# Kernel tuning notes

Measured on AMD Instinct MI355X. Metric: run time of the kernel, lower is better.

Reference implementation:

```python
import jax, jax.numpy as jnp
import numpy as np

NUM_HEAD = 16
MASKED_BIAS = -10000.0


def setup_inputs() -> dict:
    key = jax.random.key(0)
    k1, k2, k3 = jax.random.split(key, 3)
    B, M, N = 2, 2048, 1024
    x = jax.random.normal(k1, (B, M, N), dtype=jnp.float32)
    w_attn = jax.random.normal(k2, (N, 3 * N), dtype=jnp.float32) * 0.02
    w_proj = jax.random.normal(k3, (N, N), dtype=jnp.float32) * 0.02
    b_attn = jnp.zeros((3 * N,), dtype=jnp.float32)
    b_proj = jnp.zeros((N,), dtype=jnp.float32)
    return {"x": x, "w_attn": w_attn, "w_proj": w_proj,
            "b_attn": b_attn, "b_proj": b_proj}


def reference(x, w_attn, w_proj, b_attn, b_proj):
    B, M, N = x.shape
    H = NUM_HEAD
    d = N // H  # head dim
    # fused QKV projection: [B,M,3N]
    qkv = jnp.einsum('bmn,nd->bmd', x, w_attn) + b_attn
    q, k, v = jnp.split(qkv, 3, axis=-1)
    # split heads -> [B,H,M,d]
    q = q.reshape(B, M, H, d).transpose(0, 2, 1, 3)
    k = k.reshape(B, M, H, d).transpose(0, 2, 1, 3)
    v = v.reshape(B, M, H, d).transpose(0, 2, 1, 3)
    # scaled dot-product scores [B,H,M,M]
    scores = jnp.einsum('bhqd,bhkd->bhqk', q, k) / jnp.sqrt(jnp.float32(d))
    causal = jnp.tril(jnp.ones((M, M), dtype=bool))  # GPT-2 bias buffer
    scores = jnp.where(causal, scores, jnp.float32(MASKED_BIAS))
    attn = jax.nn.softmax(scores, axis=-1)
    # context [B,H,M,d] -> [B,M,N]
    ctx = jnp.einsum('bhqk,bhkd->bhqd', attn, v)
    ctx = ctx.transpose(0, 2, 1, 3).reshape(B, M, N)
    # output projection
    out = jnp.einsum('bmn,no->bmo', ctx, w_proj) + b_proj
    return out
```

## Files before the change

kernel.cpp:

```cpp
#include <hip/hip_runtime.h>

typedef __attribute__((ext_vector_type(8))) __bf16 bf16x8;
typedef __attribute__((ext_vector_type(4))) __bf16 bf16x4;
typedef __attribute__((ext_vector_type(4))) float f32x4;

__device__ __forceinline__ void async_copy16(const void* g, void* l) {
    __builtin_amdgcn_global_load_lds(
        (const __attribute__((address_space(1))) void*)g,
        (__attribute__((address_space(3))) void*)l, 16, 0, 0);
}

__global__ __launch_bounds__(256) void prep_k(
    const float* __restrict__ x, __bf16* __restrict__ xb,
    const float* __restrict__ wa, __bf16* __restrict__ wAt,
    const float* __restrict__ wp, __bf16* __restrict__ wPt)
{
    __shared__ float tile[32][33];
    const int bx = blockIdx.x;
    if (bx < 2048) {
        size_t i = ((size_t)bx * 256 + threadIdx.x) * 8;
        float4 a = *(const float4*)&x[i];
        float4 b = *(const float4*)&x[i + 4];
        bf16x8 o;
        o[0] = (__bf16)a.x; o[1] = (__bf16)a.y; o[2] = (__bf16)a.z; o[3] = (__bf16)a.w;
        o[4] = (__bf16)b.x; o[5] = (__bf16)b.y; o[6] = (__bf16)b.z; o[7] = (__bf16)b.w;
        *(bf16x8*)&xb[i] = o;
        return;
    }
    const float* src; __bf16* dst; int R, C, c0, r0;
    if (bx < 5120) {
        int id = bx - 2048;
        src = wa; dst = wAt; R = 1024; C = 3072;
        c0 = (id % 96) * 32; r0 = (id / 96) * 32;
    } else {
        int id = bx - 5120;
        src = wp; dst = wPt; R = 1024; C = 1024;
        c0 = (id & 31) * 32; r0 = (id >> 5) * 32;
    }
    int tx = threadIdx.x & 31, ty = threadIdx.x >> 5;
    for (int i = ty; i < 32; i += 8)
        tile[i][tx] = src[(size_t)(r0 + i) * C + (c0 + tx)];
    __syncthreads();
    for (int i = ty; i < 32; i += 8)
        dst[(size_t)(c0 + i) * R + (r0 + tx)] = (__bf16)tile[tx][i];
}

template <int MODE, int TN>
__global__ __launch_bounds__(256) void gemm_bt(
    const __bf16* __restrict__ A, const __bf16* __restrict__ Bt,
    const float* __restrict__ bias, int K,
    __bf16* __restrict__ O0, __bf16* __restrict__ O1, __bf16* __restrict__ O2,
    float* __restrict__ Of)
{
    constexpr int NJ = TN / 32;
    __shared__ __align__(16) __bf16 lds_a[2][128 * 32];
    __shared__ __align__(16) __bf16 lds_b[2][TN * 32];
    const int row0 = blockIdx.x * 128;
    const int col0 = blockIdx.y * TN;
    const int tid  = threadIdx.x;
    const int lane = tid & 63;
    const int w    = tid >> 6;
    const int wm   = (w >> 1) * 64, wn = (w & 1) * (TN / 2);
    const int quad = lane >> 4, l16 = lane & 15;

    auto stage = [&](int pb, int kb) {
#pragma unroll
        for (int t = 0; t < 2; ++t) {
            int s = t * 256 + tid;
            int L = s >> 3, c = (s & 7) ^ (L & 7);
            int row = 2 * L + (c >> 2), ch = c & 3;
            async_copy16(&A[(size_t)(row0 + row) * K + kb + ch * 8],
                         (char*)&lds_a[pb][0] + (t * 256 + w * 64) * 16);
        }
#pragma unroll
        for (int t = 0; t < TN / 64; ++t) {
            int s = t * 256 + tid;
            int L = s >> 3, c = (s & 7) ^ (L & 7);
            int row = 2 * L + (c >> 2), ch = c & 3;
            async_copy16(&Bt[(size_t)(col0 + row) * K + kb + ch * 8],
                         (char*)&lds_b[pb][0] + (t * 256 + w * 64) * 16);
        }
    };

    const int nIter = K >> 5;
    f32x4 acc[4][NJ] = {};
    stage(0, 0);
    for (int it = 0; it < nIter; ++it) {
        __syncthreads();
        if (it + 1 < nIter) stage((it + 1) & 1, (it + 1) << 5);
        const __bf16* la = &lds_a[it & 1][0];
        const __bf16* lb = &lds_b[it & 1][0];
        bf16x8 af[4], bfr[NJ];
#pragma unroll
        for (int i = 0; i < 4; ++i) {
            int r = wm + i * 16 + l16;
            int L = r >> 1, g = ((r & 1) * 4 + quad) ^ (L & 7);
            af[i] = *(const bf16x8*)&la[L * 64 + g * 8];
        }
#pragma unroll
        for (int j = 0; j < NJ; ++j) {
            int r = wn + j * 16 + l16;
            int L = r >> 1, g = ((r & 1) * 4 + quad) ^ (L & 7);
            bfr[j] = *(const bf16x8*)&lb[L * 64 + g * 8];
        }
#pragma unroll
        for (int i = 0; i < 4; ++i)
#pragma unroll
            for (int j = 0; j < NJ; ++j)
                acc[i][j] = __builtin_amdgcn_mfma_f32_16x16x32_bf16(
                    af[i], bfr[j], acc[i][j], 0, 0, 0);
    }

#pragma unroll
    for (int i = 0; i < 4; ++i) {
        int grow = row0 + wm + i * 16 + quad * 4;
#pragma unroll
        for (int j = 0; j < NJ; ++j) {
            int gcol = col0 + wn + j * 16 + l16;
            float bv = bias[gcol];
            if constexpr (MODE == 0) {
                int which = gcol >> 10;
                int n  = gcol & 1023;
                int hh = n >> 6, dd = n & 63;
                int bb = grow >> 11, mm0 = grow & 2047;
                int bhh = bb * 16 + hh;
                if (which == 2) {
                    int w64 = mm0 & 63;
                    int mi = (mm0 & ~63) | (w64 & 32) | ((w64 & 12) << 1)
                             | ((w64 & 16) >> 2);
                    bf16x4 pk;
#pragma unroll
                    for (int r = 0; r < 4; ++r)
                        pk[r] = (__bf16)(acc[i][j][r] + bv);
                    *(bf16x4*)&O2[((size_t)bhh * 64 + dd) * 2048 + mi] = pk;
                } else {
#pragma unroll
                    for (int r = 0; r < 4; ++r) {
                        float v = acc[i][j][r] + bv;
                        if (which == 0)
                            O0[((size_t)bhh * 2048 + mm0 + r) * 64 + dd] =
                                (__bf16)(v * 0.18033688011112042f);
                        else
                            O1[((size_t)bhh * 2048 + mm0 + r) * 64 + dd] =
                                (__bf16)v;
                    }
                }
            } else {
#pragma unroll
                for (int r = 0; r < 4; ++r) {
                    int gr = grow + r;
                    Of[(size_t)gr * 1024 + gcol] = acc[i][j][r] + bv;
                }
            }
        }
    }
}

__global__ __launch_bounds__(512, 4) void attn_kernel(
    const __bf16* __restrict__ Qh, const __bf16* __restrict__ Kh,
    const __bf16* __restrict__ Vt, __bf16* __restrict__ ctx)
{
    const int M = 2048, D = 64;
    const int bh = blockIdx.x;
    const int qt = 15 - blockIdx.y;
    const int b = bh >> 4, h = bh & 15;
    const int tid = threadIdx.x, lane = tid & 63, w = tid >> 6;
    const int quad = lane >> 4, l16 = lane & 15;

    const int q0 = qt * 128;
    const int nIter = 2 * qt + 2;

    __shared__ __align__(16) __bf16 smem[2][2][64 * 64];

    const __bf16* Qp = Qh + (size_t)bh * M * D;
    const __bf16* Kp = Kh + (size_t)bh * M * D;
    const __bf16* Vp = Vt + (size_t)bh * D * M;

    const int qw = q0 + w * 16;

    bf16x8 qf[2];
#pragma unroll
    for (int c = 0; c < 2; ++c)
        qf[c] = *(const bf16x8*)
            &Qp[(size_t)(qw + l16) * D + c * 32 + quad * 8];

    int ko[8];
#pragma unroll
    for (int t = 0; t < 4; ++t)
#pragma unroll
        for (int c = 0; c < 2; ++c) {
            int ch = ((c << 2) + quad) ^ (l16 & 7);
            ko[t * 2 + c] = (((t << 4) + l16) << 6) + (ch << 3);
        }
    int vo[8];
#pragma unroll
    for (int f = 0; f < 4; ++f)
#pragma unroll
        for (int tp = 0; tp < 2; ++tp) {
            int row = (f << 4) + l16;
            int g = ((tp << 2) + quad) ^ (row & 7);
            vo[f * 2 + tp] = (row << 6) + (g << 3);
        }

    const int cch = w * 64 + lane;
    const int srow = cch >> 3, sch = (cch & 7) ^ (srow & 7);
    const __bf16* kgp = &Kp[(size_t)srow * 64 + sch * 8];
    const __bf16* vgp = &Vp[(size_t)srow * M + sch * 8];
    char* const lbase = (char*)smem + w * 1024;

    auto stage = [&](int pb) {
        char* d = lbase + pb * 16384;
        async_copy16(kgp, d);
        async_copy16(vgp, d + 8192);
        kgp += 4096;
        vgp += 64;
    };

    f32x4 acc2[4] = {};
    f32x4 acc_s = {};
    const __bf16 onev = (__bf16)1.0f;
    const bf16x8 ones8 = {onev, onev, onev, onev, onev, onev, onev, onev};

    stage(0);

    for (int it = 0; it < nIter; ++it) {
        const int kb = it << 6;
        __syncthreads();
        if (it + 1 < nIter) stage((it + 1) & 1);
        if (kb > qw + 15) continue;
        const __bf16* kt = &smem[it & 1][0][0];
        const __bf16* vt = &smem[it & 1][1][0];

        f32x4 s[4];
        __builtin_amdgcn_s_setprio(1);
#pragma unroll
        for (int t = 0; t < 4; ++t) {
            f32x4 tt = {};
#pragma unroll
            for (int c = 0; c < 2; ++c) {
                bf16x8 kf = *(const bf16x8*)(kt + ko[t * 2 + c]);
                tt = __builtin_amdgcn_mfma_f32_16x16x32_bf16(
                    kf, qf[c], tt, 0, 0, 0);
            }
            s[t] = tt;
        }
        __builtin_amdgcn_s_setprio(0);
        if (kb + 63 > qw) {
#pragma unroll
            for (int t = 0; t < 4; ++t)
#pragma unroll
                for (int r = 0; r < 4; ++r)
                    if (kb + t * 16 + quad * 4 + r > qw + l16)
                        s[t][r] = -1e30f;
        }
        bf16x8 pf32[2];
#pragma unroll
        for (int tp = 0; tp < 2; ++tp) {
            bf16x8 pp;
#pragma unroll
            for (int r = 0; r < 4; ++r) {
                pp[r]     = (__bf16)exp2f(s[2 * tp][r]);
                pp[4 + r] = (__bf16)exp2f(s[2 * tp + 1][r]);
            }
            pf32[tp] = pp;
        }
        __builtin_amdgcn_s_setprio(1);
#pragma unroll
        for (int f = 0; f < 4; ++f) {
#pragma unroll
            for (int tp = 0; tp < 2; ++tp) {
                bf16x8 vv = *(const bf16x8*)(vt + vo[f * 2 + tp]);
                acc2[f] = __builtin_amdgcn_mfma_f32_16x16x32_bf16(
                    vv, pf32[tp], acc2[f], 0, 0, 0);
            }
        }
#pragma unroll
        for (int tp = 0; tp < 2; ++tp)
            acc_s = __builtin_amdgcn_mfma_f32_16x16x32_bf16(
                ones8, pf32[tp], acc_s, 0, 0, 0);
        __builtin_amdgcn_s_setprio(0);
    }

    __syncthreads();
    __bf16* ldsT = (__bf16*)smem;
    const float rinv = 1.0f / acc_s[0];
#pragma unroll
    for (int f = 0; f < 4; ++f) {
        bf16x4 ov;
#pragma unroll
        for (int r = 0; r < 4; ++r)
            ov[r] = (__bf16)(acc2[f][r] * rinv);
        *(bf16x4*)&ldsT[(w * 16 + l16) * 72 + f * 16 + quad * 4] = ov;
    }
    __syncthreads();
    {
        int qq = tid >> 2;
        int dp = (tid & 3) * 16;
        const __bf16* src = &ldsT[qq * 72 + dp];
        __bf16* dst = &ctx[((size_t)(b * 2048 + q0 + qq)) * 1024 + h * 64 + dp];
        *(bf16x8*)&dst[0] = *(const bf16x8*)&src[0];
        *(bf16x8*)&dst[8] = *(const bf16x8*)&src[8];
    }
}

extern "C" void kernel_launch(void* const* d_in, const int* in_sizes, int n_in,
                              void* d_out, int out_size, void* d_ws, size_t ws_size,
                              hipStream_t stream) {
    const float* x      = (const float*)d_in[0];
    const float* w_attn = (const float*)d_in[1];
    const float* w_proj = (const float*)d_in[2];
    const float* b_attn = (const float*)d_in[3];
    const float* b_proj = (const float*)d_in[4];
    float* out = (float*)d_out;

    char* ws = (char*)d_ws;
    __bf16* xb  = (__bf16*)(ws);
    __bf16* ctx = (__bf16*)(ws);
    __bf16* wAt = (__bf16*)(ws + 8388608);
    __bf16* wPt = (__bf16*)(ws + 14680064);
    __bf16* Vt  = (__bf16*)(ws + 16777216);
    __bf16* Qh  = (__bf16*)d_out;
    __bf16* Kh  = (__bf16*)d_out + 4194304;

    prep_k<<<6144, 256, 0, stream>>>(x, xb, w_attn, wAt, w_proj, wPt);
    gemm_bt<0, 128><<<dim3(32, 24), 256, 0, stream>>>(xb, wAt, b_attn, 1024,
                                                      Qh, Kh, Vt, nullptr);
    attn_kernel<<<dim3(32, 16), 512, 0, stream>>>(Qh, Kh, Vt, ctx);
    gemm_bt<1, 64><<<dim3(32, 16), 256, 0, stream>>>(ctx, wPt, b_proj, 1024,
                                                     nullptr, nullptr, nullptr, out);
}
```

Before: 174.3 us.

## Pair short and long causal query tiles per block for balanced attention work

Each attention block now handles two 64-row query tiles, y and 31-y, with 256 threads. It runs one 33-step K/V streaming loop that serves tile A first and then restarts the K/V pointers for tile B. This gives every block the same amount of causal work and removes the tail imbalance of the earlier 128-row tiles that went from heavy to light. It also swaps exp2f for the raw hardware exp2 builtin. In exchange, blocks are half as wide, so each K/V tile is reused by fewer queries. There is also an extra epilogue pass, and the builtin may handle denormals and edge cases differently.

```diff
diff --git a/kernel.cpp b/kernel.cpp
--- a/kernel.cpp
+++ b/kernel.cpp
@@ -8,6 +8,10 @@
     __builtin_amdgcn_global_load_lds(
         (const __attribute__((address_space(1))) void*)g,
         (__attribute__((address_space(3))) void*)l, 16, 0, 0);
+}
+
+__device__ __forceinline__ float fexp2(float x) {
+    return __builtin_amdgcn_exp2f(x);
 }
 
 __global__ __launch_bounds__(256) void prep_k(
@@ -156,19 +160,21 @@
     }
 }
 
-__global__ __launch_bounds__(512, 4) void attn_kernel(
+__global__ __launch_bounds__(256) void attn_kernel(
     const __bf16* __restrict__ Qh, const __bf16* __restrict__ Kh,
     const __bf16* __restrict__ Vt, __bf16* __restrict__ ctx)
 {
     const int M = 2048, D = 64;
     const int bh = blockIdx.x;
-    const int qt = 15 - blockIdx.y;
+    const int y  = blockIdx.y;
     const int b = bh >> 4, h = bh & 15;
     const int tid = threadIdx.x, lane = tid & 63, w = tid >> 6;
     const int quad = lane >> 4, l16 = lane & 15;
 
-    const int q0 = qt * 128;
-    const int nIter = 2 * qt + 2;
+    const int nA = y + 1;
+    const int nT = 33;
+    const int qA0 = y * 64, qB0 = (31 - y) * 64;
+    const int qwA = qA0 + w * 16, qwB = qB0 + w * 16;
 
     __shared__ __align__(16) __bf16 smem[2][2][64 * 64];
 
@@ -176,13 +182,12 @@
     const __bf16* Kp = Kh + (size_t)bh * M * D;
     const __bf16* Vp = Vt + (size_t)bh * D * M;
 
-    const int qw = q0 + w * 16;
-
-    bf16x8 qf[2];
-#pragma unroll
-    for (int c = 0; c < 2; ++c)
-        qf[c] = *(const bf16x8*)
-            &Qp[(size_t)(qw + l16) * D + c * 32 + quad * 8];
+    bf16x8 qfA[2], qfB[2];
+#pragma unroll
+    for (int c = 0; c < 2; ++c) {
+        qfA[c] = *(const bf16x8*)&Qp[(size_t)(qwA + l16) * D + c * 32 + quad * 8];
+        qfB[c] = *(const bf16x8*)&Qp[(size_t)(qwB + l16) * D + c * 32 + quad * 8];
+    }
 
     int ko[8];
 #pragma unroll
@@ -202,35 +207,40 @@
             vo[f * 2 + tp] = (row << 6) + (g << 3);
         }
 
-    const int cch = w * 64 + lane;
-    const int srow = cch >> 3, sch = (cch & 7) ^ (srow & 7);
-    const __bf16* kgp = &Kp[(size_t)srow * 64 + sch * 8];
-    const __bf16* vgp = &Vp[(size_t)srow * M + sch * 8];
-    char* const lbase = (char*)smem + w * 1024;
+    const __bf16* kbase[2]; const __bf16* vbase[2];
+    const __bf16* kg[2];    const __bf16* vg[2];
+#pragma unroll
+    for (int t = 0; t < 2; ++t) {
+        int c = w * 128 + t * 64 + lane;
+        int row = c >> 3, gch = (c & 7) ^ (row & 7);
+        kbase[t] = &Kp[(size_t)row * 64 + gch * 8];
+        vbase[t] = &Vp[(size_t)row * M + gch * 8];
+        kg[t] = kbase[t]; vg[t] = vbase[t];
+    }
+    char* const lbase = (char*)smem + (w * 128) * 16;
 
     auto stage = [&](int pb) {
         char* d = lbase + pb * 16384;
-        async_copy16(kgp, d);
-        async_copy16(vgp, d + 8192);
-        kgp += 4096;
-        vgp += 64;
+#pragma unroll
+        for (int t = 0; t < 2; ++t) {
+            async_copy16(kg[t], d + t * 1024);
+            async_copy16(vg[t], d + 8192 + t * 1024);
+            kg[t] += 4096;
+            vg[t] += 64;
+        }
     };
-
-    f32x4 acc2[4] = {};
-    f32x4 acc_s = {};
+    auto resetPtrs = [&]() {
+#pragma unroll
+        for (int t = 0; t < 2; ++t) { kg[t] = kbase[t]; vg[t] = vbase[t]; }
+    };
+
+    f32x4 accA[4] = {}, accB[4] = {};
+    f32x4 acc_sA = {}, acc_sB = {};
     const __bf16 onev = (__bf16)1.0f;
     const bf16x8 ones8 = {onev, onev, onev, onev, onev, onev, onev, onev};
 
-    stage(0);
-
-    for (int it = 0; it < nIter; ++it) {
-        const int kb = it << 6;
-        __syncthreads();
-        if (it + 1 < nIter) stage((it + 1) & 1);
-        if (kb > qw + 15) continue;
-        const __bf16* kt = &smem[it & 1][0][0];
-        const __bf16* vt = &smem[it & 1][1][0];
-
+    auto compute = [&](const __bf16* kt, const __bf16* vt, int kb, int qw,
+                       const bf16x8 (&qf)[2], f32x4 (&a2)[4], f32x4& as) {
         f32x4 s[4];
         __builtin_amdgcn_s_setprio(1);
 #pragma unroll
@@ -253,16 +263,16 @@
                     if (kb + t * 16 + quad * 4 + r > qw + l16)
                         s[t][r] = -1e30f;
         }
-        bf16x8 pf32[2];
+        bf16x8 pf[2];
 #pragma unroll
         for (int tp = 0; tp < 2; ++tp) {
             bf16x8 pp;
 #pragma unroll
             for (int r = 0; r < 4; ++r) {
-                pp[r]     = (__bf16)exp2f(s[2 * tp][r]);
-                pp[4 + r] = (__bf16)exp2f(s[2 * tp + 1][r]);
+                pp[r]     = (__bf16)fexp2(s[2 * tp][r]);
+                pp[4 + r] = (__bf16)fexp2(s[2 * tp + 1][r]);
             }
-            pf32[tp] = pp;
+            pf[tp] = pp;
         }
         __builtin_amdgcn_s_setprio(1);
 #pragma unroll
@@ -270,34 +280,70 @@
 #pragma unroll
             for (int tp = 0; tp < 2; ++tp) {
                 bf16x8 vv = *(const bf16x8*)(vt + vo[f * 2 + tp]);
-                acc2[f] = __builtin_amdgcn_mfma_f32_16x16x32_bf16(
-                    vv, pf32[tp], acc2[f], 0, 0, 0);
+                a2[f] = __builtin_amdgcn_mfma_f32_16x16x32_bf16(
+                    vv, pf[tp], a2[f], 0, 0, 0);
             }
         }
 #pragma unroll
         for (int tp = 0; tp < 2; ++tp)
-            acc_s = __builtin_amdgcn_mfma_f32_16x16x32_bf16(
-                ones8, pf32[tp], acc_s, 0, 0, 0);
+            as = __builtin_amdgcn_mfma_f32_16x16x32_bf16(
+                ones8, pf[tp], as, 0, 0, 0);
         __builtin_amdgcn_s_setprio(0);
-    }
-
-    __syncthreads();
+    };
+
+    stage(0);
+    if (nA == 1) resetPtrs();
+
+    for (int it = 0; it < nT; ++it) {
+        __syncthreads();
+        int nxt = it + 1;
+        if (nxt < nT) {
+            stage(nxt & 1);
+            if (nxt + 1 == nA) resetPtrs();
+        }
+        const __bf16* kt = &smem[it & 1][0][0];
+        const __bf16* vt = &smem[it & 1][1][0];
+        if (it < nA)
+            compute(kt, vt, it * 64, qwA, qfA, accA, acc_sA);
+        else
+            compute(kt, vt, (it - nA) * 64, qwB, qfB, accB, acc_sB);
+    }
+
     __bf16* ldsT = (__bf16*)smem;
-    const float rinv = 1.0f / acc_s[0];
-#pragma unroll
-    for (int f = 0; f < 4; ++f) {
-        bf16x4 ov;
-#pragma unroll
-        for (int r = 0; r < 4; ++r)
-            ov[r] = (__bf16)(acc2[f][r] * rinv);
-        *(bf16x4*)&ldsT[(w * 16 + l16) * 72 + f * 16 + quad * 4] = ov;
-    }
+    const int qq = tid >> 2;
+    const int dp = (tid & 3) * 16;
+
     __syncthreads();
     {
-        int qq = tid >> 2;
-        int dp = (tid & 3) * 16;
+        const float rinv = 1.0f / acc_sA[0];
+#pragma unroll
+        for (int f = 0; f < 4; ++f) {
+            bf16x4 ov;
+#pragma unroll
+            for (int r = 0; r < 4; ++r)
+                ov[r] = (__bf16)(accA[f][r] * rinv);
+            *(bf16x4*)&ldsT[(w * 16 + l16) * 72 + f * 16 + quad * 4] = ov;
+        }
+        __syncthreads();
         const __bf16* src = &ldsT[qq * 72 + dp];
-        __bf16* dst = &ctx[((size_t)(b * 2048 + q0 + qq)) * 1024 + h * 64 + dp];
+        __bf16* dst = &ctx[((size_t)(b * 2048 + qA0 + qq)) * 1024 + h * 64 + dp];
+        *(bf16x8*)&dst[0] = *(const bf16x8*)&src[0];
+        *(bf16x8*)&dst[8] = *(const bf16x8*)&src[8];
+    }
+    __syncthreads();
+    {
+        const float rinv = 1.0f / acc_sB[0];
+#pragma unroll
+        for (int f = 0; f < 4; ++f) {
+            bf16x4 ov;
+#pragma unroll
+            for (int r = 0; r < 4; ++r)
+                ov[r] = (__bf16)(accB[f][r] * rinv);
+            *(bf16x4*)&ldsT[(w * 16 + l16) * 72 + f * 16 + quad * 4] = ov;
+        }
+        __syncthreads();
+        const __bf16* src = &ldsT[qq * 72 + dp];
+        __bf16* dst = &ctx[((size_t)(b * 2048 + qB0 + qq)) * 1024 + h * 64 + dp];
         *(bf16x8*)&dst[0] = *(const bf16x8*)&src[0];
         *(bf16x8*)&dst[8] = *(const bf16x8*)&src[8];
     }
@@ -325,7 +371,7 @@
     prep_k<<<6144, 256, 0, stream>>>(x, xb, w_attn, wAt, w_proj, wPt);
     gemm_bt<0, 128><<<dim3(32, 24), 256, 0, stream>>>(xb, wAt, b_attn, 1024,
                                                       Qh, Kh, Vt, nullptr);
-    attn_kernel<<<dim3(32, 16), 512, 0, stream>>>(Qh, Kh, Vt, ctx);
+    attn_kernel<<<dim3(32, 16), 256, 0, stream>>>(Qh, Kh, Vt, ctx);
     gemm_bt<1, 64><<<dim3(32, 16), 256, 0, stream>>>(ctx, wPt, b_proj, 1024,
                                                      nullptr, nullptr, nullptr, out);
 }
```

After: 173.7 us, median of 2. About the same (-0.4%).

## Process two 16-row query slabs per wave to reuse K/V LDS fragments

Applied to the files above, without the earlier changes.

The attention kernel drops from 8 to 4 waves per block, and each wave now handles 32 query rows as two 16-row sub-tiles. Each K and V fragment read from LDS is reused across both sub-tiles, halving LDS reads per MFMA. Staging is rebalanced so each thread issues two async copies per matrix, and exp2f is replaced by the raw hardware exp2 builtin. The cost is higher register pressure, fewer waves to hide latency, and coarser causal skipping, since a wave only skips a K tile when all 32 of its rows are masked.

```diff
diff --git a/kernel.cpp b/kernel.cpp
--- a/kernel.cpp
+++ b/kernel.cpp
@@ -8,6 +8,10 @@
     __builtin_amdgcn_global_load_lds(
         (const __attribute__((address_space(1))) void*)g,
         (__attribute__((address_space(3))) void*)l, 16, 0, 0);
+}
+
+__device__ __forceinline__ float fexp2(float x) {
+    return __builtin_amdgcn_exp2f(x);
 }
 
 __global__ __launch_bounds__(256) void prep_k(
@@ -156,7 +160,7 @@
     }
 }
 
-__global__ __launch_bounds__(512, 4) void attn_kernel(
+__global__ __launch_bounds__(256) void attn_kernel(
     const __bf16* __restrict__ Qh, const __bf16* __restrict__ Kh,
     const __bf16* __restrict__ Vt, __bf16* __restrict__ ctx)
 {
@@ -168,7 +172,8 @@
     const int quad = lane >> 4, l16 = lane & 15;
 
     const int q0 = qt * 128;
-    const int nIter = 2 * qt + 2;
+    const int nT = 2 * qt + 2;
+    const int qw = q0 + w * 32;
 
     __shared__ __align__(16) __bf16 smem[2][2][64 * 64];
 
@@ -176,13 +181,13 @@
     const __bf16* Kp = Kh + (size_t)bh * M * D;
     const __bf16* Vp = Vt + (size_t)bh * D * M;
 
-    const int qw = q0 + w * 16;
-
-    bf16x8 qf[2];
-#pragma unroll
-    for (int c = 0; c < 2; ++c)
-        qf[c] = *(const bf16x8*)
-            &Qp[(size_t)(qw + l16) * D + c * 32 + quad * 8];
+    bf16x8 qf[2][2];
+#pragma unroll
+    for (int s = 0; s < 2; ++s)
+#pragma unroll
+        for (int c = 0; c < 2; ++c)
+            qf[s][c] = *(const bf16x8*)
+                &Qp[(size_t)(qw + s * 16 + l16) * D + c * 32 + quad * 8];
 
     int ko[8];
 #pragma unroll
@@ -202,104 +207,130 @@
             vo[f * 2 + tp] = (row << 6) + (g << 3);
         }
 
-    const int cch = w * 64 + lane;
-    const int srow = cch >> 3, sch = (cch & 7) ^ (srow & 7);
-    const __bf16* kgp = &Kp[(size_t)srow * 64 + sch * 8];
-    const __bf16* vgp = &Vp[(size_t)srow * M + sch * 8];
-    char* const lbase = (char*)smem + w * 1024;
+    const __bf16* kg[2]; const __bf16* vg[2];
+#pragma unroll
+    for (int t = 0; t < 2; ++t) {
+        int c = w * 128 + t * 64 + lane;
+        int row = c >> 3, gch = (c & 7) ^ (row & 7);
+        kg[t] = &Kp[(size_t)row * 64 + gch * 8];
+        vg[t] = &Vp[(size_t)row * M + gch * 8];
+    }
+    char* const lbase = (char*)smem + (w * 128) * 16;
 
     auto stage = [&](int pb) {
         char* d = lbase + pb * 16384;
-        async_copy16(kgp, d);
-        async_copy16(vgp, d + 8192);
-        kgp += 4096;
-        vgp += 64;
+#pragma unroll
+        for (int t = 0; t < 2; ++t) {
+            async_copy16(kg[t], d + t * 1024);
+            async_copy16(vg[t], d + 8192 + t * 1024);
+            kg[t] += 4096;
+            vg[t] += 64;
+        }
     };
 
-    f32x4 acc2[4] = {};
-    f32x4 acc_s = {};
+    f32x4 acc2[2][4] = {};
+    f32x4 acc_s[2] = {};
     const __bf16 onev = (__bf16)1.0f;
     const bf16x8 ones8 = {onev, onev, onev, onev, onev, onev, onev, onev};
 
     stage(0);
 
-    for (int it = 0; it < nIter; ++it) {
+    for (int it = 0; it < nT; ++it) {
         const int kb = it << 6;
         __syncthreads();
-        if (it + 1 < nIter) stage((it + 1) & 1);
-        if (kb > qw + 15) continue;
+        if (it + 1 < nT) stage((it + 1) & 1);
+        if (kb > qw + 31) continue;
         const __bf16* kt = &smem[it & 1][0][0];
         const __bf16* vt = &smem[it & 1][1][0];
 
-        f32x4 s[4];
+        f32x4 ss[2][4];
         __builtin_amdgcn_s_setprio(1);
 #pragma unroll
         for (int t = 0; t < 4; ++t) {
-            f32x4 tt = {};
-#pragma unroll
-            for (int c = 0; c < 2; ++c) {
-                bf16x8 kf = *(const bf16x8*)(kt + ko[t * 2 + c]);
+            bf16x8 kf0 = *(const bf16x8*)(kt + ko[t * 2 + 0]);
+            bf16x8 kf1 = *(const bf16x8*)(kt + ko[t * 2 + 1]);
+#pragma unroll
+            for (int s = 0; s < 2; ++s) {
+                f32x4 tt = {};
                 tt = __builtin_amdgcn_mfma_f32_16x16x32_bf16(
-                    kf, qf[c], tt, 0, 0, 0);
-            }
-            s[t] = tt;
+                    kf0, qf[s][0], tt, 0, 0, 0);
+                tt = __builtin_amdgcn_mfma_f32_16x16x32_bf16(
+                    kf1, qf[s][1], tt, 0, 0, 0);
+                ss[s][t] = tt;
+            }
         }
         __builtin_amdgcn_s_setprio(0);
-        if (kb + 63 > qw) {
-#pragma unroll
-            for (int t = 0; t < 4; ++t)
-#pragma unroll
-                for (int r = 0; r < 4; ++r)
-                    if (kb + t * 16 + quad * 4 + r > qw + l16)
-                        s[t][r] = -1e30f;
-        }
-        bf16x8 pf32[2];
-#pragma unroll
-        for (int tp = 0; tp < 2; ++tp) {
-            bf16x8 pp;
-#pragma unroll
-            for (int r = 0; r < 4; ++r) {
-                pp[r]     = (__bf16)exp2f(s[2 * tp][r]);
-                pp[4 + r] = (__bf16)exp2f(s[2 * tp + 1][r]);
-            }
-            pf32[tp] = pp;
-        }
+#pragma unroll
+        for (int s = 0; s < 2; ++s) {
+            int qws = qw + s * 16;
+            if (kb + 63 > qws) {
+#pragma unroll
+                for (int t = 0; t < 4; ++t)
+#pragma unroll
+                    for (int r = 0; r < 4; ++r)
+                        if (kb + t * 16 + quad * 4 + r > qws + l16)
+                            ss[s][t][r] = -1e30f;
+            }
+        }
+        bf16x8 pf[2][2];
+#pragma unroll
+        for (int s = 0; s < 2; ++s)
+#pragma unroll
+            for (int tp = 0; tp < 2; ++tp) {
+                bf16x8 pp;
+#pragma unroll
+                for (int r = 0; r < 4; ++r) {
+                    pp[r]     = (__bf16)fexp2(ss[s][2 * tp][r]);
+                    pp[4 + r] = (__bf16)fexp2(ss[s][2 * tp + 1][r]);
+                }
+                pf[s][tp] = pp;
+            }
         __builtin_amdgcn_s_setprio(1);
 #pragma unroll
         for (int f = 0; f < 4; ++f) {
-#pragma unroll
-            for (int tp = 0; tp < 2; ++tp) {
-                bf16x8 vv = *(const bf16x8*)(vt + vo[f * 2 + tp]);
-                acc2[f] = __builtin_amdgcn_mfma_f32_16x16x32_bf16(
-                    vv, pf32[tp], acc2[f], 0, 0, 0);
-            }
-        }
-#pragma unroll
-        for (int tp = 0; tp < 2; ++tp)
-            acc_s = __builtin_amdgcn_mfma_f32_16x16x32_bf16(
-                ones8, pf32[tp], acc_s, 0, 0, 0);
+            bf16x8 vv0 = *(const bf16x8*)(vt + vo[f * 2 + 0]);
+            bf16x8 vv1 = *(const bf16x8*)(vt + vo[f * 2 + 1]);
+#pragma unroll
+            for (int s = 0; s < 2; ++s) {
+                acc2[s][f] = __builtin_amdgcn_mfma_f32_16x16x32_bf16(
+                    vv0, pf[s][0], acc2[s][f], 0, 0, 0);
+                acc2[s][f] = __builtin_amdgcn_mfma_f32_16x16x32_bf16(
+                    vv1, pf[s][1], acc2[s][f], 0, 0, 0);
+            }
+        }
+#pragma unroll
+        for (int s = 0; s < 2; ++s)
+#pragma unroll
+            for (int tp = 0; tp < 2; ++tp)
+                acc_s[s] = __builtin_amdgcn_mfma_f32_16x16x32_bf16(
+                    ones8, pf[s][tp], acc_s[s], 0, 0, 0);
         __builtin_amdgcn_s_setprio(0);
     }
 
     __syncthreads();
     __bf16* ldsT = (__bf16*)smem;
-    const float rinv = 1.0f / acc_s[0];
-#pragma unroll
-    for (int f = 0; f < 4; ++f) {
-        bf16x4 ov;
-#pragma unroll
-        for (int r = 0; r < 4; ++r)
-            ov[r] = (__bf16)(acc2[f][r] * rinv);
-        *(bf16x4*)&ldsT[(w * 16 + l16) * 72 + f * 16 + quad * 4] = ov;
+#pragma unroll
+    for (int s = 0; s < 2; ++s) {
+        const float rinv = 1.0f / acc_s[s][0];
+#pragma unroll
+        for (int f = 0; f < 4; ++f) {
+            bf16x4 ov;
+#pragma unroll
+            for (int r = 0; r < 4; ++r)
+                ov[r] = (__bf16)(acc2[s][f][r] * rinv);
+            *(bf16x4*)&ldsT[(w * 32 + s * 16 + l16) * 72 + f * 16 + quad * 4] = ov;
+        }
     }
     __syncthreads();
     {
-        int qq = tid >> 2;
-        int dp = (tid & 3) * 16;
+        int qq = tid >> 1;
+        int dp = (tid & 1) * 32;
         const __bf16* src = &ldsT[qq * 72 + dp];
         __bf16* dst = &ctx[((size_t)(b * 2048 + q0 + qq)) * 1024 + h * 64 + dp];
-        *(bf16x8*)&dst[0] = *(const bf16x8*)&src[0];
-        *(bf16x8*)&dst[8] = *(const bf16x8*)&src[8];
+        *(bf16x8*)&dst[0]  = *(const bf16x8*)&src[0];
+        *(bf16x8*)&dst[8]  = *(const bf16x8*)&src[8];
+        *(bf16x8*)&dst[16] = *(const bf16x8*)&src[16];
+        *(bf16x8*)&dst[24] = *(const bf16x8*)&src[24];
     }
 }
 
@@ -325,7 +356,7 @@
     prep_k<<<6144, 256, 0, stream>>>(x, xb, w_attn, wAt, w_proj, wPt);
     gemm_bt<0, 128><<<dim3(32, 24), 256, 0, stream>>>(xb, wAt, b_attn, 1024,
                                                       Qh, Kh, Vt, nullptr);
-    attn_kernel<<<dim3(32, 16), 512, 0, stream>>>(Qh, Kh, Vt, ctx);
+    attn_kernel<<<dim3(32, 16), 256, 0, stream>>>(Qh, Kh, Vt, ctx);
     gemm_bt<1, 64><<<dim3(32, 16), 256, 0, stream>>>(ctx, wPt, b_proj, 1024,
                                                      nullptr, nullptr, nullptr, out);
 }
```

Result: no change. 174.5 us (+0.1%).
